# Performance work log

Measured on AMD Instinct MI355X. Metric: run time of the kernel, lower is better.

The kernel has to match this reference:

```python
import jax, jax.numpy as jnp
import numpy as np

B, H, L, N, COND = 8, 128, 16384, 16, 4  # N = s4_hidden_size // 2 complex states (conjugate symmetry)
BN_EPS = 1e-5


def setup_inputs() -> dict:
    key = jax.random.key(0)
    ks = jax.random.split(key, 12)
    x = jax.random.normal(ks[0], (B, H, L), jnp.float32)
    conditional_information = jax.random.normal(ks[1], (B, COND), jnp.float32)
    # input linear (H -> H)
    lin_w = jax.random.normal(ks[2], (H, H), jnp.float32) / np.sqrt(H)
    lin_b = jnp.zeros((H,), jnp.float32)
    prelu1_a = jnp.array(0.25, jnp.float32)
    # S4D (diag) parameters, ZOH discretization, S4D-Lin init
    u = jax.random.uniform(ks[3], (H,), jnp.float32)
    log_dt = np.log(1e-3) + u * (np.log(1e-1) - np.log(1e-3))  # [H]
    log_A_real = jnp.log(0.5 * jnp.ones((H, N), jnp.float32))
    A_imag = jnp.broadcast_to(np.pi * jnp.arange(N, dtype=jnp.float32), (H, N)).copy()
    C_re = jax.random.normal(ks[4], (H, N), jnp.float32)
    C_im = jax.random.normal(ks[5], (H, N), jnp.float32)
    D = jax.random.normal(ks[6], (H,), jnp.float32)
    out_w = jax.random.normal(ks[7], (H, H), jnp.float32) / np.sqrt(H)
    out_b = jnp.zeros((H,), jnp.float32)
    # FiLM: cond -> (gamma, beta) per channel
    film_w = jax.random.normal(ks[8], (2 * H, COND), jnp.float32) / np.sqrt(COND)
    film_b = jnp.zeros((2 * H,), jnp.float32)
    prelu2_a = jnp.array(0.25, jnp.float32)
    # depthwise 1x1 conv residual: per-channel scale
    res_w = jax.random.normal(ks[9], (H,), jnp.float32) / np.sqrt(H)
    return dict(x=x, conditional_information=conditional_information,
                lin_w=lin_w, lin_b=lin_b, prelu1_a=prelu1_a,
                log_dt=log_dt, log_A_real=log_A_real, A_imag=A_imag,
                C_re=C_re, C_im=C_im, D=D, out_w=out_w, out_b=out_b,
                film_w=film_w, film_b=film_b, prelu2_a=prelu2_a, res_w=res_w)


def _prelu(v, a):
    return jnp.where(v > 0, v, a * v)


def _s4d(u, log_dt, log_A_real, A_imag, C_re, C_im, D, out_w, out_b):
    # u: [B, H, L]. Diagonal SSM kernel via Vandermonde + FFT convolution (ZOH).
    Lx = u.shape[-1]
    dt = jnp.exp(log_dt)                                   # [H]
    A = -jnp.exp(log_A_real) + 1j * A_imag                 # [H, N] complex
    dtA = dt[:, None] * A                                  # [H, N]
    dB = (jnp.exp(dtA) - 1.0) / A                          # ZOH: (e^{dtA}-1)/A, B=1
    Ceff = (C_re + 1j * C_im) * dB                         # [H, N]
    t = jnp.arange(Lx, dtype=jnp.float32)
    vand = jnp.exp(dtA[:, :, None] * t)                    # [H, N, L] = (e^{dtA})^l
    K = 2.0 * jnp.real(jnp.einsum('hn,hnl->hl', Ceff, vand))  # [H, L]
    n = 2 * Lx
    y = jnp.fft.irfft(jnp.fft.rfft(u, n) * jnp.fft.rfft(K, n)[None], n)[..., :Lx]
    y = y + D[None, :, None] * u
    # position-wise output linear (activation='id')
    return jnp.einsum('bhl,gh->bgl', y, out_w) + out_b[None, :, None]


def reference(x, conditional_information, lin_w, lin_b, prelu1_a,
              log_dt, log_A_real, A_imag, C_re, C_im, D, out_w, out_b,
              film_w, film_b, prelu2_a, res_w):
    out = jnp.einsum('bhl,gh->bgl', x, lin_w) + lin_b[None, :, None]
    out = _prelu(out, prelu1_a)
    out = _s4d(out, log_dt, log_A_real, A_imag, C_re, C_im, D, out_w, out_b)
    # BatchNorm1d(affine=False), training-mode statistics over (B, L)
    mean = jnp.mean(out, axis=(0, 2), keepdims=True)
    var = jnp.var(out, axis=(0, 2), keepdims=True)
    out = (out - mean) * jax.lax.rsqrt(var + BN_EPS)
    # FiLM
    gb = conditional_information @ film_w.T + film_b       # [B, 2H]
    g, b = gb[:, :H], gb[:, H:]
    out = out * g[:, :, None] + b[:, :, None]
    out = _prelu(out, prelu2_a)
    # depthwise 1x1 conv residual (groups=H, no bias): per-channel scale of x
    return out + res_w[None, :, None] * x
```

## Files before the change

kernel.cpp:

```cpp
#include <hip/hip_runtime.h>
#include <math.h>

#define B_ 8
#define H_ 128
#define L_ 16384
#define N_ 16
#define CHUNK_ 64
#define NCH_ 256

typedef float f32x4 __attribute__((ext_vector_type(4)));
typedef short bf16x8 __attribute__((ext_vector_type(8)));

static __device__ __forceinline__ unsigned int f2bf(float f) {
  unsigned int u = __float_as_uint(f);
  return (u + 0x7FFFu + ((u >> 16) & 1u)) >> 16;
}
static __device__ __forceinline__ float bf2f(unsigned int us) {
  return __uint_as_float(us << 16);
}

__global__ __launch_bounds__(256) void prep2_kernel(
    const float* __restrict__ lin_w, const float* __restrict__ out_w,
    const float* __restrict__ log_dt, const float* __restrict__ log_A_real,
    const float* __restrict__ A_imag, const float* __restrict__ C_re,
    const float* __restrict__ C_im, const float* __restrict__ cond,
    const float* __restrict__ film_w, const float* __restrict__ film_b,
    unsigned short* __restrict__ wA16, unsigned short* __restrict__ wB16,
    float* __restrict__ consts,
    float* __restrict__ gact, float* __restrict__ bact)
{
  int blk = blockIdx.x, t = threadIdx.x;
  if (blk < 16) {
    int base = blk * 1024;
    #pragma unroll
    for (int it = 0; it < 4; it++) {
      int i = base + it * 256 + t;
      wA16[i] = (unsigned short)f2bf(lin_w[i]);
      wB16[i] = (unsigned short)f2bf(out_w[i]);
    }
  } else if (blk == 16) {
    for (int i = t; i < H_ * N_; i += 256) {
      int h = i >> 4, n = i & 15;
      float dt  = expf(log_dt[h]);
      float Are = -expf(log_A_real[i]);
      float Aim = A_imag[i];
      float dre = dt * Are, dim = dt * Aim;
      float er  = expf(dre);
      float wre = er * cosf(dim);
      float wim = er * sinf(dim);
      float den = Are * Are + Aim * Aim;
      float nre = wre - 1.0f, nim = wim;
      float dBre = (nre * Are + nim * Aim) / den;
      float dBim = (nim * Are - nre * Aim) / den;
      float cr = C_re[i], ci = C_im[i];
      float cere = cr * dBre - ci * dBim;
      float ceim = cr * dBim + ci * dBre;
      float e2   = expf((float)CHUNK_ * dre);
      float wcre = e2 * cosf((float)CHUNK_ * dim);
      float wcim = e2 * sinf((float)CHUNK_ * dim);
      float* cb = consts + h * 96;
      cb[n]      = wre;  cb[16 + n] = wim;
      cb[32 + n] = cere; cb[48 + n] = ceim;
      cb[64 + n] = wcre; cb[80 + n] = wcim;
    }
  } else {
    for (int i = t; i < B_ * 2 * H_; i += 256) {
      int b = i >> 8, k = i & 255;
      float acc = film_b[k];
      #pragma unroll
      for (int c = 0; c < 4; c++) acc += cond[b * 4 + c] * film_w[k * 4 + c];
      if (k < H_) gact[b * H_ + k] = acc;
      else        bact[b * H_ + (k - H_)] = acc;
    }
  }
}

template<int MODE>
__global__ __launch_bounds__(256) void mgemm_kernel(
    const void* inv, const unsigned short* __restrict__ w16,
    const float* __restrict__ bias, const float* __restrict__ prelu_a,
    unsigned short* __restrict__ outb)
{
  __shared__ __align__(16) unsigned short xT[128 * 128];
  char* xb = (char*)xT;
  int tid = threadIdx.x;
  int blk = blockIdx.x;
  int b   = blk >> 7;
  int jb  = (blk & 127) << 7;

  {
    int hp = tid >> 4;
    int jq = tid & 15;
    int h0 = hp << 3;
    int j0 = jq << 3;
    if (MODE == 0) {
      const float* inb = (const float*)inv + ((size_t)b * H_) * L_ + jb;
      f32x4 r[8][2];
      #pragma unroll
      for (int rr = 0; rr < 8; rr++) {
        r[rr][0] = *reinterpret_cast<const f32x4*>(&inb[(size_t)(h0 + rr) * L_ + j0]);
        r[rr][1] = *reinterpret_cast<const f32x4*>(&inb[(size_t)(h0 + rr) * L_ + j0 + 4]);
      }
      #pragma unroll
      for (int jj = 0; jj < 8; jj++) {
        int j = j0 + jj;
        uint4 pk;
        #define GE_(rr) ((jj < 4) ? r[rr][0][jj] : r[rr][1][jj - 4])
        pk.x = f2bf(GE_(0)) | (f2bf(GE_(1)) << 16);
        pk.y = f2bf(GE_(2)) | (f2bf(GE_(3)) << 16);
        pk.z = f2bf(GE_(4)) | (f2bf(GE_(5)) << 16);
        pk.w = f2bf(GE_(6)) | (f2bf(GE_(7)) << 16);
        #undef GE_
        int addr = j * 256 + ((hp << 4) ^ ((j & 15) << 4));
        *reinterpret_cast<uint4*>(xb + addr) = pk;
      }
    } else {
      const unsigned short* ub = (const unsigned short*)inv;
      uint4 rv[8];
      #pragma unroll
      for (int rr = 0; rr < 8; rr++)
        rv[rr] = *reinterpret_cast<const uint4*>(
            ub + ((size_t)(b * H_ + h0 + rr)) * 32768 + jb + j0);
      #pragma unroll
      for (int jj = 0; jj < 8; jj++) {
        int j = j0 + jj;
        uint4 pk;
        #define WD_(rr) ((jj >> 1) == 0 ? rv[rr].x : (jj >> 1) == 1 ? rv[rr].y : \
                         (jj >> 1) == 2 ? rv[rr].z : rv[rr].w)
        #define EXT_(rr) (((jj & 1) ? (WD_(rr) >> 16) : WD_(rr)) & 0xFFFFu)
        pk.x = EXT_(0) | (EXT_(1) << 16);
        pk.y = EXT_(2) | (EXT_(3) << 16);
        pk.z = EXT_(4) | (EXT_(5) << 16);
        pk.w = EXT_(6) | (EXT_(7) << 16);
        #undef EXT_
        #undef WD_
        int addr = j * 256 + ((hp << 4) ^ ((j & 15) << 4));
        *reinterpret_cast<uint4*>(xb + addr) = pk;
      }
    }
  }
  __syncthreads();

  int lane = tid & 63;
  int w    = tid >> 6;
  int wg   = w >> 1;
  int wj   = w & 1;
  int ln   = lane & 15;
  int q    = lane >> 4;
  f32x4 acc[4][4];
  #pragma unroll
  for (int mi = 0; mi < 4; mi++)
    #pragma unroll
    for (int n = 0; n < 4; n++) acc[mi][n] = (f32x4)0.0f;

  #pragma unroll
  for (int kb = 0; kb < 4; kb++) {
    bf16x8 a[4], bv[4];
    #pragma unroll
    for (int mi = 0; mi < 4; mi++)
      a[mi] = *reinterpret_cast<const bf16x8*>(
          &w16[(size_t)(wg * 64 + mi * 16 + ln) * 128 + kb * 32 + q * 8]);
    #pragma unroll
    for (int n = 0; n < 4; n++) {
      int jl = wj * 64 + n * 16 + ln;
      int ar = jl * 256 + (((kb << 6) + (q << 4)) ^ ((jl & 15) << 4));
      bv[n] = *reinterpret_cast<bf16x8*>(xb + ar);
    }
    #pragma unroll
    for (int mi = 0; mi < 4; mi++)
      #pragma unroll
      for (int n = 0; n < 4; n++)
        acc[mi][n] = __builtin_amdgcn_mfma_f32_16x16x32_bf16(a[mi], bv[n], acc[mi][n], 0, 0, 0);
  }

  float pa = (MODE == 0) ? prelu_a[0] : 0.0f;
  #pragma unroll
  for (int mi = 0; mi < 4; mi++) {
    #pragma unroll
    for (int r = 0; r < 4; r++) {
      int g = wg * 64 + mi * 16 + q * 4 + r;
      float bvs = bias[g];
      size_t orow = ((size_t)(b * H_ + g)) * 32768 + jb + wj * 64 + ln;
      #pragma unroll
      for (int n = 0; n < 4; n++) {
        float v = acc[mi][n][r] + bvs;
        if (MODE == 0) v = (v > 0.0f) ? v : pa * v;
        outb[orow + n * 16] = (unsigned short)f2bf(v);
      }
    }
  }
}

__global__ __launch_bounds__(1024) void scan4_kernel(
    unsigned short* ub, const float* __restrict__ consts, const float* __restrict__ Dp)
{
  __shared__ unsigned int rowl[8192];
  __shared__ float agg[16][32];
  int tid = threadIdx.x;
  int row = blockIdx.x;
  int h   = row & 127;
  const float* cb = consts + h * 96;
  unsigned int* grow = (unsigned int*)ub + (size_t)row * 16384;

  #pragma unroll
  for (int rd = 0; rd < 2; rd++) {
    int u0   = rd * 4096 + tid * 4;
    uint4 v  = *reinterpret_cast<const uint4*>(grow + u0);
    int phys = u0 ^ (((u0 >> 5) & 7) << 2);
    *reinterpret_cast<uint4*>(&rowl[phys]) = v;
  }
  __syncthreads();

  int c     = tid >> 2;
  int m     = tid & 3;
  int lane  = tid & 63;
  int cl    = lane >> 2;
  int wv    = tid >> 6;
  int cbase = c * 32;
  int swz   = (c & 7) << 2;

  float wre[4], wim[4];
  #pragma unroll
  for (int k = 0; k < 4; k++) { wre[k] = cb[4*m+k]; wim[k] = cb[16+4*m+k]; }

  float sre[4] = {0.f,0.f,0.f,0.f}, sim[4] = {0.f,0.f,0.f,0.f};

  #define UPD_(uval) { \
    _Pragma("unroll") \
    for (int k = 0; k < 4; k++) { \
      float nr = fmaf(wre[k], sre[k], fmaf(-wim[k], sim[k], (uval))); \
      float ni = fmaf(wre[k], sim[k], wim[k] * sre[k]); \
      sre[k] = nr; sim[k] = ni; } }

  for (int e2 = 0; e2 < 16; e2++) {
    int idx  = (cbase + 2 * e2) ^ swz;
    uint2 pv = *reinterpret_cast<uint2*>(&rowl[idx]);
    float u0 = __uint_as_float(pv.x << 16);
    float u1 = __uint_as_float(pv.x & 0xFFFF0000u);
    float u2 = __uint_as_float(pv.y << 16);
    float u3 = __uint_as_float(pv.y & 0xFFFF0000u);
    UPD_(u0); UPD_(u1); UPD_(u2); UPD_(u3);
  }

  float mre[4], mim[4];
  #pragma unroll
  for (int k = 0; k < 4; k++) { mre[k] = cb[64+4*m+k]; mim[k] = cb[80+4*m+k]; }
  float pwr[4] = {1.f,1.f,1.f,1.f}, pwi[4] = {0.f,0.f,0.f,0.f};
  #pragma unroll
  for (int s = 0; s < 4; s++) {
    int off = 1 << s;
    bool bit = (cl >> s) & 1;
    #pragma unroll
    for (int k = 0; k < 4; k++) {
      float tr = fmaf(pwr[k], mre[k], -(pwi[k] * mim[k]));
      float ti = fmaf(pwr[k], mim[k],  (pwi[k] * mre[k]));
      pwr[k] = bit ? tr : pwr[k];
      pwi[k] = bit ? ti : pwi[k];
    }
    bool act = (cl >= off);
    #pragma unroll
    for (int k = 0; k < 4; k++) {
      float pr = __shfl_up(sre[k], 4 * off, 64);
      float pi = __shfl_up(sim[k], 4 * off, 64);
      float nr = fmaf(mre[k], pr, fmaf(-mim[k], pi, sre[k]));
      float ni = fmaf(mre[k], pi, fmaf( mim[k], pr, sim[k]));
      sre[k] = act ? nr : sre[k];
      sim[k] = act ? ni : sim[k];
    }
    #pragma unroll
    for (int k = 0; k < 4; k++) {
      float r = mre[k], i2 = mim[k];
      mre[k] = fmaf(r, r, -(i2 * i2));
      mim[k] = 2.0f * r * i2;
    }
  }

  if (cl == 15) {
    #pragma unroll
    for (int k = 0; k < 4; k++) {
      agg[wv][m * 8 + 2 * k]     = sre[k];
      agg[wv][m * 8 + 2 * k + 1] = sim[k];
    }
  }
  __syncthreads();
  float Cr[4] = {0.f,0.f,0.f,0.f}, Ci[4] = {0.f,0.f,0.f,0.f};
  for (int wp = 0; wp < wv; wp++) {
    #pragma unroll
    for (int k = 0; k < 4; k++) {
      float ar = agg[wp][m * 8 + 2 * k];
      float ai = agg[wp][m * 8 + 2 * k + 1];
      float nr = fmaf(mre[k], Cr[k], fmaf(-mim[k], Ci[k], ar));
      float ni = fmaf(mre[k], Ci[k], fmaf( mim[k], Cr[k], ai));
      Cr[k] = nr; Ci[k] = ni;
    }
  }

  #pragma unroll
  for (int k = 0; k < 4; k++) {
    float er = __shfl_up(sre[k], 4, 64);
    float ei = __shfl_up(sim[k], 4, 64);
    float br = (cl == 0) ? 0.0f : er;
    float bi = (cl == 0) ? 0.0f : ei;
    sre[k] = fmaf(pwr[k], Cr[k], fmaf(-pwi[k], Ci[k], br));
    sim[k] = fmaf(pwr[k], Ci[k], fmaf( pwi[k], Cr[k], bi));
  }

  float cre[4], cim[4];
  #pragma unroll
  for (int k = 0; k < 4; k++) { cre[k] = cb[32+4*m+k]; cim[k] = cb[48+4*m+k]; }
  float Dv = Dp[h];

  #define STEP_(uval, yout) { \
    float ya = 0.0f; \
    _Pragma("unroll") \
    for (int k = 0; k < 4; k++) { \
      float nr = fmaf(wre[k], sre[k], fmaf(-wim[k], sim[k], (uval))); \
      float ni = fmaf(wre[k], sim[k], wim[k] * sre[k]); \
      sre[k] = nr; sim[k] = ni; \
      ya = fmaf(cre[k], nr, fmaf(-cim[k], ni, ya)); } \
    yout = ya; }

  for (int e2 = 0; e2 < 16; e2++) {
    int idx  = (cbase + 2 * e2) ^ swz;
    uint2 pv = *reinterpret_cast<uint2*>(&rowl[idx]);
    float u0 = __uint_as_float(pv.x << 16);
    float u1 = __uint_as_float(pv.x & 0xFFFF0000u);
    float u2 = __uint_as_float(pv.y << 16);
    float u3 = __uint_as_float(pv.y & 0xFFFF0000u);
    float y0, y1, y2, y3;
    STEP_(u0, y0); STEP_(u1, y1); STEP_(u2, y2); STEP_(u3, y3);
    y0 += __shfl_xor(y0, 1); y0 += __shfl_xor(y0, 2);
    y1 += __shfl_xor(y1, 1); y1 += __shfl_xor(y1, 2);
    y2 += __shfl_xor(y2, 1); y2 += __shfl_xor(y2, 2);
    y3 += __shfl_xor(y3, 1); y3 += __shfl_xor(y3, 2);
    if (m == 0) {
      y0 = fmaf(Dv, u0, 2.0f * y0);
      y1 = fmaf(Dv, u1, 2.0f * y1);
      y2 = fmaf(Dv, u2, 2.0f * y2);
      y3 = fmaf(Dv, u3, 2.0f * y3);
      uint2 pk;
      pk.x = f2bf(y0) | (f2bf(y1) << 16);
      pk.y = f2bf(y2) | (f2bf(y3) << 16);
      *reinterpret_cast<uint2*>(&rowl[idx]) = pk;
    }
  }
  #undef UPD_
  #undef STEP_
  __syncthreads();

  #pragma unroll
  for (int rd = 0; rd < 2; rd++) {
    int u0   = rd * 4096 + tid * 4;
    int phys = u0 ^ (((u0 >> 5) & 7) << 2);
    uint4 v  = *reinterpret_cast<const uint4*>(&rowl[phys]);
    *reinterpret_cast<uint4*>(grow + u0) = v;
  }
}

__global__ __launch_bounds__(256) void stats1_kernel(
    const unsigned short* __restrict__ ub,
    float* __restrict__ sums, float* __restrict__ sumsq)
{
  int row = blockIdx.x, tid = threadIdx.x;
  const unsigned int* zr = (const unsigned int*)ub + (size_t)row * 16384;
  float s1 = 0.0f, s2 = 0.0f;
  #pragma unroll
  for (int rd = 0; rd < 8; rd++) {
    uint4 v = *reinterpret_cast<const uint4*>(zr + rd * 1024 + tid * 4);
    unsigned int ws_[4] = {v.x, v.y, v.z, v.w};
    #pragma unroll
    for (int k = 0; k < 4; k++) {
      float f0 = bf2f(ws_[k] & 0xFFFFu), f1 = bf2f(ws_[k] >> 16);
      s1 += f0 + f1;
      s2 = fmaf(f0, f0, fmaf(f1, f1, s2));
    }
  }
  #pragma unroll
  for (int off = 1; off < 64; off <<= 1) {
    s1 += __shfl_xor(s1, off);
    s2 += __shfl_xor(s2, off);
  }
  __shared__ float a1[4], a2[4];
  int wv = tid >> 6;
  if ((tid & 63) == 0) { a1[wv] = s1; a2[wv] = s2; }
  __syncthreads();
  if (tid == 0) {
    sums[row]  = a1[0] + a1[1] + a1[2] + a1[3];
    sumsq[row] = a2[0] + a2[1] + a2[2] + a2[3];
  }
}

__global__ void stats2_kernel(const float* __restrict__ sums,
                              const float* __restrict__ sumsq,
                              float* __restrict__ meanp, float* __restrict__ invp)
{
  int g = threadIdx.x;
  if (g < H_) {
    double s1 = 0.0, s2 = 0.0;
    #pragma unroll
    for (int b = 0; b < B_; b++) {
      s1 += (double)sums[b * H_ + g];
      s2 += (double)sumsq[b * H_ + g];
    }
    double cnt = (double)B_ * (double)L_;
    double mu  = s1 / cnt;
    double var = s2 / cnt - mu * mu;
    meanp[g] = (float)mu;
    invp[g]  = (float)(1.0 / sqrt(var + 1e-5));
  }
}

__global__ __launch_bounds__(256) void final2_kernel(
    unsigned short* __restrict__ ub, float* __restrict__ outf,
    const float* __restrict__ x,
    const float* __restrict__ meanp, const float* __restrict__ invp,
    const float* __restrict__ gact, const float* __restrict__ bact,
    const float* __restrict__ prelu2_a, const float* __restrict__ res_w)
{
  int row = blockIdx.x, tid = threadIdx.x;
  int b = row >> 7, g = row & 127;
  const unsigned int* zr = (const unsigned int*)ub + (size_t)row * 16384;
  uint4 zq0 = *reinterpret_cast<const uint4*>(zr + 0 * 1024 + tid * 4);
  uint4 zq1 = *reinterpret_cast<const uint4*>(zr + 1 * 1024 + tid * 4);
  uint4 zq2 = *reinterpret_cast<const uint4*>(zr + 2 * 1024 + tid * 4);
  uint4 zq3 = *reinterpret_cast<const uint4*>(zr + 3 * 1024 + tid * 4);
  uint4 zq4 = *reinterpret_cast<const uint4*>(zr + 4 * 1024 + tid * 4);
  uint4 zq5 = *reinterpret_cast<const uint4*>(zr + 5 * 1024 + tid * 4);
  uint4 zq6 = *reinterpret_cast<const uint4*>(zr + 6 * 1024 + tid * 4);
  uint4 zq7 = *reinterpret_cast<const uint4*>(zr + 7 * 1024 + tid * 4);
  __syncthreads();

  float m  = meanp[g], iv = invp[g];
  float ga = gact[b * H_ + g], bb = bact[b * H_ + g];
  float rw = res_w[g], pa = prelu2_a[0];
  const float* xr = x + (size_t)row * L_;
  float* orow = outf + (size_t)row * L_;

  uint4 zqa[8] = {zq0, zq1, zq2, zq3, zq4, zq5, zq6, zq7};
  #pragma unroll
  for (int rd = 0; rd < 8; rd++) {
    int e0 = rd * 2048 + tid * 8;
    f32x4 x0 = *reinterpret_cast<const f32x4*>(xr + e0);
    f32x4 x1 = *reinterpret_cast<const f32x4*>(xr + e0 + 4);
    unsigned int wz[4] = {zqa[rd].x, zqa[rd].y, zqa[rd].z, zqa[rd].w};
    f32x4 o0, o1;
    #pragma unroll
    for (int k = 0; k < 4; k++) {
      float z0 = bf2f(wz[k] & 0xFFFFu), z1 = bf2f(wz[k] >> 16);
      float v0 = fmaf((z0 - m) * iv, ga, bb);
      float v1 = fmaf((z1 - m) * iv, ga, bb);
      v0 = (v0 > 0.0f) ? v0 : pa * v0;
      v1 = (v1 > 0.0f) ? v1 : pa * v1;
      float xa = (k < 2) ? x0[2 * k] : x1[2 * k - 4];
      float xbv = (k < 2) ? x0[2 * k + 1] : x1[2 * k - 3];
      float r0 = fmaf(rw, xa, v0);
      float r1 = fmaf(rw, xbv, v1);
      if (k < 2) { o0[2 * k] = r0; o0[2 * k + 1] = r1; }
      else       { o1[2 * k - 4] = r0; o1[2 * k - 3] = r1; }
    }
    *reinterpret_cast<f32x4*>(orow + e0)     = o0;
    *reinterpret_cast<f32x4*>(orow + e0 + 4) = o1;
  }
}

extern "C" void kernel_launch(void* const* d_in, const int* in_sizes, int n_in,
                              void* d_out, int out_size, void* d_ws, size_t ws_size,
                              hipStream_t stream)
{
  const float* x        = (const float*)d_in[0];
  const float* cond     = (const float*)d_in[1];
  const float* lin_w    = (const float*)d_in[2];
  const float* lin_b    = (const float*)d_in[3];
  const float* prelu1_a = (const float*)d_in[4];
  const float* log_dt   = (const float*)d_in[5];
  const float* log_A    = (const float*)d_in[6];
  const float* A_imag   = (const float*)d_in[7];
  const float* C_re     = (const float*)d_in[8];
  const float* C_im     = (const float*)d_in[9];
  const float* Dp       = (const float*)d_in[10];
  const float* out_w    = (const float*)d_in[11];
  const float* out_b    = (const float*)d_in[12];
  const float* film_w   = (const float*)d_in[13];
  const float* film_b   = (const float*)d_in[14];
  const float* prelu2_a = (const float*)d_in[15];
  const float* res_w    = (const float*)d_in[16];
  float* outf = (float*)d_out;
  unsigned short* ubuf = (unsigned short*)d_out;

  char* wsb = (char*)d_ws;
  float* consts         = (float*)(wsb + 0);
  unsigned short* wA16  = (unsigned short*)(wsb + 49152);
  unsigned short* wB16  = (unsigned short*)(wsb + 81920);
  float* gact           = (float*)(wsb + 114688);
  float* bact           = (float*)(wsb + 118784);
  float* meanp          = (float*)(wsb + 122880);
  float* invp           = (float*)(wsb + 123392);
  float* sums           = (float*)(wsb + 123904);
  float* sumsq          = (float*)(wsb + 128000);

  prep2_kernel<<<18, 256, 0, stream>>>(lin_w, out_w, log_dt, log_A, A_imag, C_re, C_im,
                                       cond, film_w, film_b, wA16, wB16, consts, gact, bact);
  mgemm_kernel<0><<<1024, 256, 0, stream>>>(x, wA16, lin_b, prelu1_a, ubuf);
  scan4_kernel<<<1024, 1024, 0, stream>>>(ubuf, consts, Dp);
  mgemm_kernel<1><<<1024, 256, 0, stream>>>(ubuf, wB16, out_b, nullptr, ubuf);
  stats1_kernel<<<1024, 256, 0, stream>>>(ubuf, sums, sumsq);
  stats2_kernel<<<1, 128, 0, stream>>>(sums, sumsq, meanp, invp);
  final2_kernel<<<1024, 256, 0, stream>>>(ubuf, outf, x, meanp, invp, gact, bact,
                                          prelu2_a, res_w);
}
```

Before: 314.6 us.

## Fuse BatchNorm statistics into output GEMM epilogue and vectorize scan LDS reads

Accumulates per-channel sum and sum-of-squares inside the second GEMM epilogue, first within the block via shuffles and shared atomics and then through global atomics. This removes the separate stats pass over the bf16 buffer and one kernel launch. It also switches bf16 packing to the hardware v_cvt_pk_bf16_f32 instruction and v_perm, and widens the scan's LDS reads to 128-bit loads with software prefetch. In exchange it adds global atomic contention, makes the float sums order-dependent, and computes stats from pre-rounding values rather than the stored bf16 values.

Result: slower. 360.8 us (+14.7%).

```diff
diff --git a/kernel.cpp b/kernel.cpp
--- a/kernel.cpp
+++ b/kernel.cpp
@@ -17,6 +17,11 @@
 }
 static __device__ __forceinline__ float bf2f(unsigned int us) {
   return __uint_as_float(us << 16);
+}
+static __device__ __forceinline__ unsigned int cvtpk(float lo, float hi) {
+  unsigned int r;
+  asm("v_cvt_pk_bf16_f32 %0, %1, %2" : "=v"(r) : "v"(lo), "v"(hi));
+  return r;
 }
 
 __global__ __launch_bounds__(256) void prep2_kernel(
@@ -27,7 +32,8 @@
     const float* __restrict__ film_w, const float* __restrict__ film_b,
     unsigned short* __restrict__ wA16, unsigned short* __restrict__ wB16,
     float* __restrict__ consts,
-    float* __restrict__ gact, float* __restrict__ bact)
+    float* __restrict__ gact, float* __restrict__ bact,
+    float* __restrict__ bnsum, float* __restrict__ bnsumsq)
 {
   int blk = blockIdx.x, t = threadIdx.x;
   if (blk < 16) {
@@ -63,6 +69,8 @@
       cb[32 + n] = cere; cb[48 + n] = ceim;
       cb[64 + n] = wcre; cb[80 + n] = wcim;
     }
+    if (t < 128) bnsum[t] = 0.0f;
+    else         bnsumsq[t - 128] = 0.0f;
   } else {
     for (int i = t; i < B_ * 2 * H_; i += 256) {
       int b = i >> 8, k = i & 255;
@@ -79,14 +87,18 @@
 __global__ __launch_bounds__(256) void mgemm_kernel(
     const void* inv, const unsigned short* __restrict__ w16,
     const float* __restrict__ bias, const float* __restrict__ prelu_a,
-    unsigned short* __restrict__ outb)
+    unsigned short* __restrict__ outb,
+    float* __restrict__ bnsum, float* __restrict__ bnsumsq)
 {
   __shared__ __align__(16) unsigned short xT[128 * 128];
+  __shared__ float bs1[128], bs2[128];
   char* xb = (char*)xT;
   int tid = threadIdx.x;
   int blk = blockIdx.x;
   int b   = blk >> 7;
   int jb  = (blk & 127) << 7;
+
+  if (MODE == 1 && tid < 128) { bs1[tid] = 0.0f; bs2[tid] = 0.0f; }
 
   {
     int hp = tid >> 4;
@@ -106,10 +118,10 @@
         int j = j0 + jj;
         uint4 pk;
         #define GE_(rr) ((jj < 4) ? r[rr][0][jj] : r[rr][1][jj - 4])
-        pk.x = f2bf(GE_(0)) | (f2bf(GE_(1)) << 16);
-        pk.y = f2bf(GE_(2)) | (f2bf(GE_(3)) << 16);
-        pk.z = f2bf(GE_(4)) | (f2bf(GE_(5)) << 16);
-        pk.w = f2bf(GE_(6)) | (f2bf(GE_(7)) << 16);
+        pk.x = cvtpk(GE_(0), GE_(1));
+        pk.y = cvtpk(GE_(2), GE_(3));
+        pk.z = cvtpk(GE_(4), GE_(5));
+        pk.w = cvtpk(GE_(6), GE_(7));
         #undef GE_
         int addr = j * 256 + ((hp << 4) ^ ((j & 15) << 4));
         *reinterpret_cast<uint4*>(xb + addr) = pk;
@@ -124,15 +136,14 @@
       #pragma unroll
       for (int jj = 0; jj < 8; jj++) {
         int j = j0 + jj;
+        unsigned int sel = (jj & 1) ? 0x07060302u : 0x05040100u;
         uint4 pk;
         #define WD_(rr) ((jj >> 1) == 0 ? rv[rr].x : (jj >> 1) == 1 ? rv[rr].y : \
                          (jj >> 1) == 2 ? rv[rr].z : rv[rr].w)
-        #define EXT_(rr) (((jj & 1) ? (WD_(rr) >> 16) : WD_(rr)) & 0xFFFFu)
-        pk.x = EXT_(0) | (EXT_(1) << 16);
-        pk.y = EXT_(2) | (EXT_(3) << 16);
-        pk.z = EXT_(4) | (EXT_(5) << 16);
-        pk.w = EXT_(6) | (EXT_(7) << 16);
-        #undef EXT_
+        pk.x = __builtin_amdgcn_perm(WD_(1), WD_(0), sel);
+        pk.y = __builtin_amdgcn_perm(WD_(3), WD_(2), sel);
+        pk.z = __builtin_amdgcn_perm(WD_(5), WD_(4), sel);
+        pk.w = __builtin_amdgcn_perm(WD_(7), WD_(6), sel);
         #undef WD_
         int addr = j * 256 + ((hp << 4) ^ ((j & 15) << 4));
         *reinterpret_cast<uint4*>(xb + addr) = pk;
@@ -181,12 +192,32 @@
       int g = wg * 64 + mi * 16 + q * 4 + r;
       float bvs = bias[g];
       size_t orow = ((size_t)(b * H_ + g)) * 32768 + jb + wj * 64 + ln;
+      float s1 = 0.0f, s2 = 0.0f;
       #pragma unroll
       for (int n = 0; n < 4; n++) {
         float v = acc[mi][n][r] + bvs;
         if (MODE == 0) v = (v > 0.0f) ? v : pa * v;
         outb[orow + n * 16] = (unsigned short)f2bf(v);
-      }
+        if (MODE == 1) { s1 += v; s2 = fmaf(v, v, s2); }
+      }
+      if (MODE == 1) {
+        #pragma unroll
+        for (int off = 1; off < 16; off <<= 1) {
+          s1 += __shfl_xor(s1, off);
+          s2 += __shfl_xor(s2, off);
+        }
+        if (ln == 0) {
+          atomicAdd(&bs1[g], s1);
+          atomicAdd(&bs2[g], s2);
+        }
+      }
+    }
+  }
+  if (MODE == 1) {
+    __syncthreads();
+    if (tid < 128) {
+      atomicAdd(&bnsum[tid], bs1[tid]);
+      atomicAdd(&bnsumsq[tid], bs2[tid]);
     }
   }
 }
@@ -194,7 +225,7 @@
 __global__ __launch_bounds__(1024) void scan4_kernel(
     unsigned short* ub, const float* __restrict__ consts, const float* __restrict__ Dp)
 {
-  __shared__ unsigned int rowl[8192];
+  __shared__ __align__(16) unsigned int rowl[8192];
   __shared__ float agg[16][32];
   int tid = threadIdx.x;
   int row = blockIdx.x;
@@ -232,14 +263,21 @@
       float ni = fmaf(wre[k], sim[k], wim[k] * sre[k]); \
       sre[k] = nr; sim[k] = ni; } }
 
-  for (int e2 = 0; e2 < 16; e2++) {
-    int idx  = (cbase + 2 * e2) ^ swz;
-    uint2 pv = *reinterpret_cast<uint2*>(&rowl[idx]);
-    float u0 = __uint_as_float(pv.x << 16);
-    float u1 = __uint_as_float(pv.x & 0xFFFF0000u);
-    float u2 = __uint_as_float(pv.y << 16);
-    float u3 = __uint_as_float(pv.y & 0xFFFF0000u);
-    UPD_(u0); UPD_(u1); UPD_(u2); UPD_(u3);
+  {
+    uint4 pv = *reinterpret_cast<uint4*>(&rowl[cbase ^ swz]);
+    #pragma unroll
+    for (int e4 = 0; e4 < 8; e4++) {
+      uint4 nxt = pv;
+      if (e4 < 7) nxt = *reinterpret_cast<uint4*>(&rowl[(cbase + 4 * (e4 + 1)) ^ swz]);
+      unsigned int wd[4] = {pv.x, pv.y, pv.z, pv.w};
+      #pragma unroll
+      for (int p = 0; p < 4; p++) {
+        float u0 = __uint_as_float(wd[p] << 16);
+        float u1 = __uint_as_float(wd[p] & 0xFFFF0000u);
+        UPD_(u0); UPD_(u1);
+      }
+      pv = nxt;
+    }
   }
 
   float mre[4], mim[4];
@@ -320,28 +358,30 @@
       ya = fmaf(cre[k], nr, fmaf(-cim[k], ni, ya)); } \
     yout = ya; }
 
-  for (int e2 = 0; e2 < 16; e2++) {
-    int idx  = (cbase + 2 * e2) ^ swz;
-    uint2 pv = *reinterpret_cast<uint2*>(&rowl[idx]);
-    float u0 = __uint_as_float(pv.x << 16);
-    float u1 = __uint_as_float(pv.x & 0xFFFF0000u);
-    float u2 = __uint_as_float(pv.y << 16);
-    float u3 = __uint_as_float(pv.y & 0xFFFF0000u);
-    float y0, y1, y2, y3;
-    STEP_(u0, y0); STEP_(u1, y1); STEP_(u2, y2); STEP_(u3, y3);
-    y0 += __shfl_xor(y0, 1); y0 += __shfl_xor(y0, 2);
-    y1 += __shfl_xor(y1, 1); y1 += __shfl_xor(y1, 2);
-    y2 += __shfl_xor(y2, 1); y2 += __shfl_xor(y2, 2);
-    y3 += __shfl_xor(y3, 1); y3 += __shfl_xor(y3, 2);
-    if (m == 0) {
-      y0 = fmaf(Dv, u0, 2.0f * y0);
-      y1 = fmaf(Dv, u1, 2.0f * y1);
-      y2 = fmaf(Dv, u2, 2.0f * y2);
-      y3 = fmaf(Dv, u3, 2.0f * y3);
-      uint2 pk;
-      pk.x = f2bf(y0) | (f2bf(y1) << 16);
-      pk.y = f2bf(y2) | (f2bf(y3) << 16);
-      *reinterpret_cast<uint2*>(&rowl[idx]) = pk;
+  {
+    uint4 pv = *reinterpret_cast<uint4*>(&rowl[cbase ^ swz]);
+    #pragma unroll
+    for (int e4 = 0; e4 < 8; e4++) {
+      int idx = (cbase + 4 * e4) ^ swz;
+      uint4 nxt = pv;
+      if (e4 < 7) nxt = *reinterpret_cast<uint4*>(&rowl[(cbase + 4 * (e4 + 1)) ^ swz]);
+      unsigned int wd[4] = {pv.x, pv.y, pv.z, pv.w};
+      unsigned int po[4];
+      #pragma unroll
+      for (int p = 0; p < 4; p++) {
+        float u0 = __uint_as_float(wd[p] << 16);
+        float u1 = __uint_as_float(wd[p] & 0xFFFF0000u);
+        float y0, y1;
+        STEP_(u0, y0); STEP_(u1, y1);
+        y0 += __shfl_xor(y0, 1); y0 += __shfl_xor(y0, 2);
+        y1 += __shfl_xor(y1, 1); y1 += __shfl_xor(y1, 2);
+        y0 = fmaf(Dv, u0, 2.0f * y0);
+        y1 = fmaf(Dv, u1, 2.0f * y1);
+        po[p] = cvtpk(y0, y1);
+      }
+      if (m == 0)
+        *reinterpret_cast<uint4*>(&rowl[idx]) = make_uint4(po[0], po[1], po[2], po[3]);
+      pv = nxt;
     }
   }
   #undef UPD_
@@ -357,54 +397,15 @@
   }
 }
 
-__global__ __launch_bounds__(256) void stats1_kernel(
-    const unsigned short* __restrict__ ub,
-    float* __restrict__ sums, float* __restrict__ sumsq)
-{
-  int row = blockIdx.x, tid = threadIdx.x;
-  const unsigned int* zr = (const unsigned int*)ub + (size_t)row * 16384;
-  float s1 = 0.0f, s2 = 0.0f;
-  #pragma unroll
-  for (int rd = 0; rd < 8; rd++) {
-    uint4 v = *reinterpret_cast<const uint4*>(zr + rd * 1024 + tid * 4);
-    unsigned int ws_[4] = {v.x, v.y, v.z, v.w};
-    #pragma unroll
-    for (int k = 0; k < 4; k++) {
-      float f0 = bf2f(ws_[k] & 0xFFFFu), f1 = bf2f(ws_[k] >> 16);
-      s1 += f0 + f1;
-      s2 = fmaf(f0, f0, fmaf(f1, f1, s2));
-    }
-  }
-  #pragma unroll
-  for (int off = 1; off < 64; off <<= 1) {
-    s1 += __shfl_xor(s1, off);
-    s2 += __shfl_xor(s2, off);
-  }
-  __shared__ float a1[4], a2[4];
-  int wv = tid >> 6;
-  if ((tid & 63) == 0) { a1[wv] = s1; a2[wv] = s2; }
-  __syncthreads();
-  if (tid == 0) {
-    sums[row]  = a1[0] + a1[1] + a1[2] + a1[3];
-    sumsq[row] = a2[0] + a2[1] + a2[2] + a2[3];
-  }
-}
-
-__global__ void stats2_kernel(const float* __restrict__ sums,
-                              const float* __restrict__ sumsq,
-                              float* __restrict__ meanp, float* __restrict__ invp)
+__global__ void bnfinal_kernel(const float* __restrict__ bnsum,
+                               const float* __restrict__ bnsumsq,
+                               float* __restrict__ meanp, float* __restrict__ invp)
 {
   int g = threadIdx.x;
   if (g < H_) {
-    double s1 = 0.0, s2 = 0.0;
-    #pragma unroll
-    for (int b = 0; b < B_; b++) {
-      s1 += (double)sums[b * H_ + g];
-      s2 += (double)sumsq[b * H_ + g];
-    }
     double cnt = (double)B_ * (double)L_;
-    double mu  = s1 / cnt;
-    double var = s2 / cnt - mu * mu;
+    double mu  = (double)bnsum[g] / cnt;
+    double var = (double)bnsumsq[g] / cnt - mu * mu;
     meanp[g] = (float)mu;
     invp[g]  = (float)(1.0 / sqrt(var + 1e-5));
   }
@@ -495,16 +496,18 @@
   float* bact           = (float*)(wsb + 118784);
   float* meanp          = (float*)(wsb + 122880);
   float* invp           = (float*)(wsb + 123392);
-  float* sums           = (float*)(wsb + 123904);
-  float* sumsq          = (float*)(wsb + 128000);
+  float* bnsum          = (float*)(wsb + 123904);
+  float* bnsumsq        = (float*)(wsb + 124416);
 
   prep2_kernel<<<18, 256, 0, stream>>>(lin_w, out_w, log_dt, log_A, A_imag, C_re, C_im,
-                                       cond, film_w, film_b, wA16, wB16, consts, gact, bact);
-  mgemm_kernel<0><<<1024, 256, 0, stream>>>(x, wA16, lin_b, prelu1_a, ubuf);
+                                       cond, film_w, film_b, wA16, wB16, consts, gact, bact,
+                                       bnsum, bnsumsq);
+  mgemm_kernel<0><<<1024, 256, 0, stream>>>(x, wA16, lin_b, prelu1_a, ubuf,
+                                            nullptr, nullptr);
   scan4_kernel<<<1024, 1024, 0, stream>>>(ubuf, consts, Dp);
-  mgemm_kernel<1><<<1024, 256, 0, stream>>>(ubuf, wB16, out_b, nullptr, ubuf);
-  stats1_kernel<<<1024, 256, 0, stream>>>(ubuf, sums, sumsq);
-  stats2_kernel<<<1, 128, 0, stream>>>(sums, sumsq, meanp, invp);
+  mgemm_kernel<1><<<1024, 256, 0, stream>>>(ubuf, wB16, out_b, nullptr, ubuf,
+                                            bnsum, bnsumsq);
+  bnfinal_kernel<<<1, 128, 0, stream>>>(bnsum, bnsumsq, meanp, invp);
   final2_kernel<<<1024, 256, 0, stream>>>(ubuf, outf, x, meanp, invp, gact, bact,
                                           prelu2_a, res_w);
 }
```
